# Optimization experiments

Hardware: AMD Instinct MI355X
Metric: run time of the kernel (lower is better)

## Reference

```python
import jax, jax.numpy as jnp
import numpy as np

L = 4            # n_layers
D_MODEL = 768
D_STATE = 16
D_CONV = 4
EXPAND = 2
D_INNER = EXPAND * D_MODEL      # 1536
DT_RANK = (D_MODEL + 15) // 16  # 48
B = 2
T = 2048
LN_EPS = 1e-5


def setup_inputs() -> dict:
    key = jax.random.key(0)
    ks = jax.random.split(key, 12)
    s = 0.02
    x = jax.random.normal(ks[0], (B, T, D_MODEL), dtype=jnp.float32)
    in_proj_w = jax.random.normal(ks[1], (L, 2 * D_INNER, D_MODEL), dtype=jnp.float32) * s
    conv_w = jax.random.normal(ks[2], (L, D_INNER, D_CONV), dtype=jnp.float32) * s
    conv_b = jnp.zeros((L, D_INNER), dtype=jnp.float32)
    x_proj_w = jax.random.normal(ks[3], (L, DT_RANK + 2 * D_STATE, D_INNER), dtype=jnp.float32) * s
    dt_proj_w = jax.random.normal(ks[4], (L, D_INNER, DT_RANK), dtype=jnp.float32) * s
    dt_proj_b = jax.random.normal(ks[5], (L, D_INNER), dtype=jnp.float32) * 0.1
    # Standard S4D-real init: A = -[1..d_state], stored as log
    A_log = jnp.log(jnp.broadcast_to(
        jnp.arange(1, D_STATE + 1, dtype=jnp.float32), (L, D_INNER, D_STATE)))
    D_param = jnp.ones((L, D_INNER), dtype=jnp.float32)
    out_proj_w = jax.random.normal(ks[6], (L, D_MODEL, D_INNER), dtype=jnp.float32) * s
    ln_g = jnp.ones((L, D_MODEL), dtype=jnp.float32)
    ln_b = jnp.zeros((L, D_MODEL), dtype=jnp.float32)
    return {"x": x, "in_proj_w": in_proj_w, "conv_w": conv_w, "conv_b": conv_b,
            "x_proj_w": x_proj_w, "dt_proj_w": dt_proj_w, "dt_proj_b": dt_proj_b,
            "A_log": A_log, "D_param": D_param, "out_proj_w": out_proj_w,
            "ln_g": ln_g, "ln_b": ln_b}


def _layernorm(x, g, b):
    mu = jnp.mean(x, axis=-1, keepdims=True)
    var = jnp.mean(jnp.square(x - mu), axis=-1, keepdims=True)
    return (x - mu) * jax.lax.rsqrt(var + LN_EPS) * g + b


def _mamba_layer(x, inw, convw, convb, xpw, dtw, dtb, A_log, Dp, outw):
    # x: [B,T,d_model]
    Tn = x.shape[1]
    xz = jnp.einsum('btd,ed->bte', x, inw)          # [B,T,2*d_inner]
    xin, z = jnp.split(xz, 2, axis=-1)              # each [B,T,d_inner]
    # causal depthwise conv1d over time (kernel d_conv)
    xp = jnp.pad(xin, ((0, 0), (D_CONV - 1, 0), (0, 0)))
    xc = convb
    for k in range(D_CONV):
        xc = xc + xp[:, k:k + Tn, :] * convw[:, k]
    xc = jax.nn.silu(xc)                            # [B,T,d_inner]
    dbl = jnp.einsum('bti,ei->bte', xc, xpw)        # [B,T,dt_rank+2*d_state]
    dt, Bs, Cs = jnp.split(dbl, [DT_RANK, DT_RANK + D_STATE], axis=-1)
    dt = jax.nn.softplus(jnp.einsum('btr,dr->btd', dt, dtw) + dtb)  # [B,T,d_inner]
    A = -jnp.exp(A_log)                             # [d_inner,d_state]
    dA = jnp.exp(jnp.einsum('btd,dn->btdn', dt, A))  # discretized A
    dBu = (dt * xc)[..., None] * Bs[:, :, None, :]   # [B,T,d_inner,d_state]

    def step(h, inp):
        dA_t, dBu_t, C_t = inp                      # [B,d,n],[B,d,n],[B,n]
        h = dA_t * h + dBu_t
        y = jnp.einsum('bdn,bn->bd', h, C_t)
        return h, y

    h0 = jnp.zeros((x.shape[0], D_INNER, D_STATE), x.dtype)
    _, ys = jax.lax.scan(step, h0,
                         (jnp.swapaxes(dA, 0, 1), jnp.swapaxes(dBu, 0, 1),
                          jnp.swapaxes(Cs, 0, 1)))
    y = jnp.swapaxes(ys, 0, 1) + xc * Dp            # skip connection D*u
    y = y * jax.nn.silu(z)                          # gate
    return jnp.einsum('bti,ei->bte', y, outw)       # [B,T,d_model]


def reference(x, in_proj_w, conv_w, conv_b, x_proj_w, dt_proj_w, dt_proj_b,
              A_log, D_param, out_proj_w, ln_g, ln_b):
    for l in range(L):
        residual = x
        h = _mamba_layer(x, in_proj_w[l], conv_w[l], conv_b[l], x_proj_w[l],
                         dt_proj_w[l], dt_proj_b[l], A_log[l], D_param[l],
                         out_proj_w[l])
        h = _layernorm(h, ln_g[l], ln_b[l])
        x = h + residual                            # dropout=0 -> identity
    return x
```

## Files before the change

### kernel.cpp

```cpp
#include <hip/hip_runtime.h>

#define T_LEN 2048
#define DM    768
#define DI    1536
#define DS    16
#define BB    2
#define NROWS (BB * T_LEN)
#define NCH   64
#define CLEN  32
#define NSEG  8
#define SEGC  8

#define OFF_DTB 0
#define OFF_A   6144
#define OFF_DP  104448
#define OFF_CW  110592
#define OFF_CB  135168
#define OFF_LG  141312
#define OFF_LB  144384
#define PRM_TOT 147456

typedef __attribute__((ext_vector_type(8))) short bh8;
typedef __attribute__((ext_vector_type(4))) float f32x4;

typedef const __attribute__((address_space(1))) void as1_void;
typedef __attribute__((address_space(3))) void as3_void;

__device__ __forceinline__ void glds16(const void* g, void* l) {
    __builtin_amdgcn_global_load_lds((as1_void*)g, (as3_void*)l, 16, 0, 0);
}

__device__ __forceinline__ float bf2f(unsigned short u) {
    return __uint_as_float(((unsigned)u) << 16);
}
__device__ __forceinline__ unsigned short f2bf(float f) {
    unsigned u = __float_as_uint(f);
    u += 0x7FFFu + ((u >> 16) & 1u);
    return (unsigned short)(u >> 16);
}

__device__ __forceinline__ void ld8(const void* p, long e0, int bf, float* v) {
    if (bf) {
        bh8 u = *(const bh8*)((const unsigned short*)p + e0);
#pragma unroll
        for (int j = 0; j < 8; ++j) v[j] = bf2f((unsigned short)u[j]);
    } else {
        const f32x4* q = (const f32x4*)((const float*)p + e0);
        f32x4 a = q[0], b = q[1];
#pragma unroll
        for (int j = 0; j < 4; ++j) { v[j] = a[j]; v[4 + j] = b[j]; }
    }
}

__device__ __forceinline__ void cp8(unsigned short* dst, long de0,
                                    const void* src, long se0, int bf) {
    if (bf) {
        *(bh8*)&dst[de0] = *(const bh8*)((const unsigned short*)src + se0);
    } else {
        const f32x4* q = (const f32x4*)((const float*)src + se0);
        f32x4 a = q[0], b = q[1];
        bh8 o;
#pragma unroll
        for (int j = 0; j < 4; ++j) { o[j] = (short)f2bf(a[j]); o[4 + j] = (short)f2bf(b[j]); }
        *(bh8*)&dst[de0] = o;
    }
}

__global__ void k_sniff(const unsigned short* __restrict__ x, int* __restrict__ flag) {
    __shared__ int cnt[4];
    int tid = threadIdx.x;
    int local = 0;
#pragma unroll
    for (int j = 0; j < 4; ++j) {
        unsigned short u = x[tid * 4 + j];
        int e = (u >> 7) & 0xFF;
        if (e >= 100 && e <= 140) local++;
    }
    for (int off = 32; off; off >>= 1) local += __shfl_down(local, off, 64);
    if ((tid & 63) == 0) cnt[tid >> 6] = local;
    __syncthreads();
    if (tid == 0) {
        int tot = cnt[0] + cnt[1] + cnt[2] + cnt[3];
        *flag = (tot >= 900) ? 1 : 0;
    }
}

__global__ void k_prep(const void* in_x, const void* in_inw, const void* in_ow,
                       const void* in_xpw, const void* in_dtw,
                       const void* dtb, const void* alog, const void* dpar,
                       const void* cw, const void* cb, const void* lg, const void* lb,
                       unsigned short* __restrict__ xbf, float* __restrict__ xf,
                       unsigned short* __restrict__ Win, unsigned short* __restrict__ Wout,
                       unsigned short* __restrict__ Wxp, unsigned short* __restrict__ Wdt,
                       float* __restrict__ prm, const int* __restrict__ flag) {
    const long G0 = 393216L;
    const long G1 = G0 + 1179648L;
    const long G2 = G1 + 589824L;
    const long G3 = G2 + 98304L;
    const long G4 = G3 + 49152L;
    const long G5 = G4 + 18432L;
    int bf = *flag;
    long g = (long)blockIdx.x * 256 + threadIdx.x;
    if (g >= G5) return;
    if (g < G0) {
        long e0 = g * 8;
        float v[8];
        ld8(in_x, e0, bf, v);
        bh8 o;
#pragma unroll
        for (int j = 0; j < 8; ++j) o[j] = (short)f2bf(v[j]);
        *(bh8*)&xbf[e0] = o;
        f32x4 a, b;
#pragma unroll
        for (int j = 0; j < 4; ++j) { a[j] = v[j]; b[j] = v[4 + j]; }
        ((f32x4*)&xf[e0])[0] = a;
        ((f32x4*)&xf[e0])[1] = b;
    } else if (g < G1) {
        long e0 = (g - G0) * 8;
        cp8(Win, e0, in_inw, e0, bf);
    } else if (g < G2) {
        long e0 = (g - G1) * 8;
        cp8(Wout, e0, in_ow, e0, bf);
    } else if (g < G3) {
        long e0 = (g - G2) * 8;
        int c = (int)(e0 % 1536);
        long rl = e0 / 1536;
        int r = (int)(rl % 128);
        int l = (int)(rl / 128);
        if (r < 80) cp8(Wxp, e0, in_xpw, ((long)l * 80 + r) * 1536 + c, bf);
        else        *(bh8*)&Wxp[e0] = (bh8)(short)0;
    } else if (g < G4) {
        long e0 = (g - G3) * 8;
        int c = (int)(e0 & 63);
        long rl = e0 >> 6;
        int d = (int)(rl % 1536);
        int l = (int)(rl / 1536);
        if (c < 48) cp8(Wdt, e0, in_dtw, ((long)l * 1536 + d) * 48 + c, bf);
        else        *(bh8*)&Wdt[e0] = (bh8)(short)0;
    } else {
        long e0 = (g - G4) * 8;
        float v[8];
        if (e0 < OFF_A)        ld8(dtb,  e0 - OFF_DTB, bf, v);
        else if (e0 < OFF_DP) {
            ld8(alog, e0 - OFF_A, bf, v);
#pragma unroll
            for (int j = 0; j < 8; ++j) v[j] = -__expf(v[j]);
        }
        else if (e0 < OFF_CW)  ld8(dpar, e0 - OFF_DP, bf, v);
        else if (e0 < OFF_CB)  ld8(cw,   e0 - OFF_CW, bf, v);
        else if (e0 < OFF_LG)  ld8(cb,   e0 - OFF_CB, bf, v);
        else if (e0 < OFF_LB)  ld8(lg,   e0 - OFF_LG, bf, v);
        else                   ld8(lb,   e0 - OFF_LB, bf, v);
        f32x4 a, b;
#pragma unroll
        for (int j = 0; j < 4; ++j) { a[j] = v[j]; b[j] = v[4 + j]; }
        ((f32x4*)&prm[e0])[0] = a;
        ((f32x4*)&prm[e0])[1] = b;
    }
}

template <int OUTF32>
__global__ __launch_bounds__(256) void k_gemm128(const unsigned short* __restrict__ A,
                                                 const unsigned short* __restrict__ B,
                                                 void* __restrict__ Cv,
                                                 int M, int N, int K) {
    __shared__ __align__(16) unsigned short As[128 * 32];
    __shared__ __align__(16) unsigned short Bs[128 * 32];
    const int tid = threadIdx.x;
    const int lane = tid & 63, wid = tid >> 6;
    const int wm = wid >> 1, wn = wid & 1;
    const long arow0 = (long)blockIdx.y * 128;
    const long bcol0 = (long)blockIdx.x * 128;
    const int r16 = lane >> 2;
    const int c8  = (lane & 3) * 8;
    f32x4 acc[4][4] = {};

    for (int k0 = 0; k0 < K; k0 += 32) {
#pragma unroll
        for (int j = 0; j < 2; ++j) {
            int chunk = wid + j * 4;
            int row = chunk * 16 + r16;
            glds16(&A[(arow0 + row) * K + k0 + c8], &As[chunk * 512]);
            glds16(&B[(bcol0 + row) * K + k0 + c8], &Bs[chunk * 512]);
        }
        __syncthreads();
        const int row = lane & 15, q8 = (lane >> 4) * 8;
        bh8 af[4], bfr[4];
#pragma unroll
        for (int i = 0; i < 4; ++i) af[i] = *(const bh8*)&As[(wm * 64 + i * 16 + row) * 32 + q8];
#pragma unroll
        for (int i = 0; i < 4; ++i) bfr[i] = *(const bh8*)&Bs[(wn * 64 + i * 16 + row) * 32 + q8];
#pragma unroll
        for (int i = 0; i < 4; ++i)
#pragma unroll
            for (int j = 0; j < 4; ++j)
                acc[i][j] = __builtin_amdgcn_mfma_f32_16x16x32_bf16(af[i], bfr[j], acc[i][j], 0, 0, 0);
        __syncthreads();
    }
    const int crow = (lane >> 4) * 4, ccol = lane & 15;
#pragma unroll
    for (int i = 0; i < 4; ++i)
#pragma unroll
        for (int j = 0; j < 4; ++j)
#pragma unroll
            for (int r = 0; r < 4; ++r) {
                long gr = arow0 + wm * 64 + i * 16 + crow + r;
                long gc = bcol0 + wn * 64 + j * 16 + ccol;
                if (OUTF32) ((float*)Cv)[gr * N + gc] = acc[i][j][r];
                else ((unsigned short*)Cv)[gr * N + gc] = f2bf(acc[i][j][r]);
            }
}

__global__ __launch_bounds__(256) void k_xproj(const unsigned short* __restrict__ A,
                                               const unsigned short* __restrict__ B,
                                               float* __restrict__ C) {
    __shared__ __align__(16) unsigned short As[32 * 32];
    __shared__ __align__(16) unsigned short Bs[64 * 32];
    const int tid = threadIdx.x;
    const int lane = tid & 63, w = tid >> 6;
    const int wm = w >> 1, wn = w & 1;
    const long arow0 = (long)blockIdx.y * 32;
    const long bcol0 = (long)blockIdx.x * 64;
    const int r4 = lane >> 2;
    const int c8 = (lane & 3) * 8;
    f32x4 acc[2] = {};

    for (int k0 = 0; k0 < DI; k0 += 32) {
        if (w < 2) {
            glds16(&A[(arow0 + w * 16 + r4) * DI + k0 + c8], &As[w * 512]);
            glds16(&B[(bcol0 + 32 + w * 16 + r4) * DI + k0 + c8], &Bs[1024 + w * 512]);
        } else {
            glds16(&B[(bcol0 + (w - 2) * 16 + r4) * DI + k0 + c8], &Bs[(w - 2) * 512]);
        }
        __syncthreads();
        const int row2 = lane & 15, q8 = (lane >> 4) * 8;
        bh8 af = *(const bh8*)&As[(wm * 16 + row2) * 32 + q8];
        bh8 b0 = *(const bh8*)&Bs[(wn * 32 + row2) * 32 + q8];
        bh8 b1 = *(const bh8*)&Bs[(wn * 32 + 16 + row2) * 32 + q8];
        acc[0] = __builtin_amdgcn_mfma_f32_16x16x32_bf16(af, b0, acc[0], 0, 0, 0);
        acc[1] = __builtin_amdgcn_mfma_f32_16x16x32_bf16(af, b1, acc[1], 0, 0, 0);
        __syncthreads();
    }
    const int crow = (lane >> 4) * 4, ccol = lane & 15;
#pragma unroll
    for (int j = 0; j < 2; ++j)
#pragma unroll
        for (int r = 0; r < 4; ++r) {
            long gr = arow0 + wm * 16 + crow + r;
            long gc = bcol0 + wn * 32 + j * 16 + ccol;
            C[gr * 128 + gc] = acc[j][r];
        }
}

__global__ __launch_bounds__(256) void k_dtproj(const float* __restrict__ Dbl,
                                                const unsigned short* __restrict__ Wdt,
                                                const float* __restrict__ bias,
                                                unsigned short* __restrict__ Dt) {
    __shared__ __align__(16) unsigned short As[2 * 64 * 32];
    __shared__ __align__(16) unsigned short Bs[2 * 64 * 32];
    const int tid = threadIdx.x;
    const int lane = tid & 63, wid = tid >> 6;
    const int wm = wid >> 1, wn = wid & 1;
    const long arow0 = (long)blockIdx.y * 64;
    const long bcol0 = (long)blockIdx.x * 64;

    {
        int r = tid >> 2;
        int cs = (tid & 3) * 16;
        unsigned short tmp[16];
#pragma unroll
        for (int q = 0; q < 4; ++q) {
            int col0 = cs + q * 4;
            if (col0 < 48) {
                f32x4 v = *(const f32x4*)&Dbl[(arow0 + r) * 128 + col0];
#pragma unroll
                for (int j = 0; j < 4; ++j) tmp[q * 4 + j] = f2bf(v[j]);
            } else {
#pragma unroll
                for (int j = 0; j < 4; ++j) tmp[q * 4 + j] = 0;
            }
        }
        int p = cs >> 5;
        int cp = cs & 31;
        *(bh8*)&As[p * 2048 + r * 32 + cp]     = *(bh8*)&tmp[0];
        *(bh8*)&As[p * 2048 + r * 32 + cp + 8] = *(bh8*)&tmp[8];
    }
#pragma unroll
    for (int j = 0; j < 2; ++j) {
        int chunk = tid + j * 256;
        int p = chunk >> 8;
        int rem = chunk & 255;
        int row = rem >> 2;
        int c4 = rem & 3;
        glds16(&Wdt[(bcol0 + row) * 64 + p * 32 + c4 * 8], &Bs[chunk * 8]);
    }
    __syncthreads();

    const int row2 = lane & 15, q8 = (lane >> 4) * 8;
    f32x4 acc[2][2] = {};
#pragma unroll
    for (int p = 0; p < 2; ++p) {
        bh8 af[2], bfr[2];
#pragma unroll
        for (int i = 0; i < 2; ++i) af[i] = *(const bh8*)&As[p * 2048 + (wm * 32 + i * 16 + row2) * 32 + q8];
#pragma unroll
        for (int i = 0; i < 2; ++i) bfr[i] = *(const bh8*)&Bs[p * 2048 + (wn * 32 + i * 16 + row2) * 32 + q8];
#pragma unroll
        for (int i = 0; i < 2; ++i)
#pragma unroll
            for (int j = 0; j < 2; ++j)
                acc[i][j] = __builtin_amdgcn_mfma_f32_16x16x32_bf16(af[i], bfr[j], acc[i][j], 0, 0, 0);
    }
    const int crow = (lane >> 4) * 4, ccol = lane & 15;
#pragma unroll
    for (int i = 0; i < 2; ++i)
#pragma unroll
        for (int j = 0; j < 2; ++j)
#pragma unroll
            for (int r = 0; r < 4; ++r) {
                long gr = arow0 + wm * 32 + i * 16 + crow + r;
                long gc = bcol0 + wn * 32 + j * 16 + ccol;
                float v = acc[i][j][r] + bias[gc];
                v = (v > 20.f) ? v : log1pf(__expf(v));
                Dt[gr * DI + gc] = f2bf(v);
            }
}

__global__ __launch_bounds__(256) void k_conv(const unsigned short* __restrict__ xz,
                                              const float* __restrict__ cw,
                                              const float* __restrict__ cb,
                                              unsigned short* __restrict__ xcbf) {
    __shared__ float tile[131 * 64];
    const int tid = threadIdx.x;
    const int d0 = blockIdx.x * 64;
    const long t0 = (long)blockIdx.y * 128;
    const bool seqstart = ((int)t0 & (T_LEN - 1)) == 0;
    for (int j = tid; j < 131 * 64; j += 256) {
        int row = j >> 6, col = j & 63;
        float v = 0.f;
        if (!(seqstart && row < 3)) v = bf2f(xz[(t0 - 3 + row) * (2 * DI) + d0 + col]);
        tile[j] = v;
    }
    __syncthreads();
    const int d = tid & 63, tl0 = tid >> 6;
    const int dg = d0 + d;
    const float w0 = cw[dg * 4 + 0], w1 = cw[dg * 4 + 1];
    const float w2 = cw[dg * 4 + 2], w3 = cw[dg * 4 + 3];
    const float bias = cb[dg];
    for (int tt = tl0; tt < 128; tt += 4) {
        float acc = bias + w0 * tile[tt * 64 + d] + w1 * tile[(tt + 1) * 64 + d]
                         + w2 * tile[(tt + 2) * 64 + d] + w3 * tile[(tt + 3) * 64 + d];
        float s = acc / (1.f + __expf(-acc));
        xcbf[(t0 + tt) * DI + dg] = f2bf(s);
    }
}

__global__ __launch_bounds__(256) void k_scan1(const unsigned short* __restrict__ dt,
                                               const unsigned short* __restrict__ xcbf,
                                               const float* __restrict__ dbl,
                                               const float* __restrict__ An,
                                               float* __restrict__ hch,
                                               float* __restrict__ sdtb) {
    const int tid = threadIdx.x;
    const int db = blockIdx.x % 6;
    const int c  = (blockIdx.x / 6) % NCH;
    const int b  = blockIdx.x / (6 * NCH);
    const int d  = db * 256 + tid;
    const int t0 = c * CLEN;
    float h[DS], An_r[DS];
    const f32x4* Ap = (const f32x4*)(An + (long)d * DS);
#pragma unroll
    for (int q = 0; q < 4; ++q) {
        f32x4 a4 = Ap[q];
#pragma unroll
        for (int j = 0; j < 4; ++j) { An_r[q * 4 + j] = a4[j]; h[q * 4 + j] = 0.f; }
    }
    float sdt = 0.f;
    const long rowb = (long)b * T_LEN + t0;
#pragma unroll 4
    for (int s = 0; s < CLEN; ++s) {
        long bt = rowb + s;
        float dtv = bf2f(dt[bt * DI + d]);
        float xcv = bf2f(xcbf[bt * DI + d]);
        int bi = __builtin_amdgcn_readfirstlane((int)(bt * 128 + 48));
        const f32x4* bp = (const f32x4*)(dbl + bi);
        float Bv[DS];
#pragma unroll
        for (int q = 0; q < 4; ++q) {
            f32x4 b4 = bp[q];
#pragma unroll
            for (int j = 0; j < 4; ++j) Bv[q * 4 + j] = b4[j];
        }
        float du = dtv * xcv;
        sdt += dtv;
#pragma unroll
        for (int n = 0; n < DS; ++n)
            h[n] = __expf(An_r[n] * dtv) * h[n] + du * Bv[n];
    }
    long o = (((long)b * NCH + c) * DI + d) * DS;
    f32x4* hp = (f32x4*)(hch + o);
#pragma unroll
    for (int q = 0; q < 4; ++q) {
        f32x4 h4;
#pragma unroll
        for (int j = 0; j < 4; ++j) h4[j] = h[q * 4 + j];
        hp[q] = h4;
    }
    sdtb[((long)b * NCH + c) * DI + d] = sdt;
}

__global__ __launch_bounds__(256) void k_scan2a(float* __restrict__ hbuf,
                                                const float* __restrict__ sdtb,
                                                const float* __restrict__ An,
                                                float* __restrict__ cum,
                                                float* __restrict__ Gseg,
                                                float* __restrict__ Sseg) {
    long gid = (long)blockIdx.x * 256 + threadIdx.x;
    int n = (int)(gid & 15);
    long t = gid >> 4;
    int d  = (int)(t % DI);
    int sg = (int)((t / DI) & (NSEG - 1));
    int b  = (int)(t / (DI * NSEG));
    float an = An[(long)d * DS + n];
    float h = 0.f, cs = 0.f;
    for (int i = 0; i < SEGC; ++i) {
        int c = sg * SEGC + i;
        long rowi = ((long)b * NCH + c) * DI + d;
        long idx = rowi * DS + n;
        float sdt = sdtb[rowi];
        float g = hbuf[idx];
        hbuf[idx] = h;
        if (n == 0) cum[rowi] = cs;
        h = __expf(an * sdt) * h + g;
        cs += sdt;
    }
    long gi = (((long)b * NSEG + sg) * DI + d) * DS + n;
    Gseg[gi] = h;
    if (n == 0) Sseg[((long)b * NSEG + sg) * DI + d] = cs;
}

__global__ __launch_bounds__(256) void k_scan2b(const float* __restrict__ Gseg,
                                                const float* __restrict__ Sseg,
                                                const float* __restrict__ An,
                                                float* __restrict__ Hseg) {
    long gid = (long)blockIdx.x * 256 + threadIdx.x;
    int n = (int)(gid & 15);
    long t = gid >> 4;
    int d = (int)(t % DI);
    int b = (int)(t / DI);
    float an = An[(long)d * DS + n];
    float H = 0.f;
    for (int sg = 0; sg < NSEG; ++sg) {
        long gi = (((long)b * NSEG + sg) * DI + d) * DS + n;
        float G = Gseg[gi];
        float S = Sseg[((long)b * NSEG + sg) * DI + d];
        Hseg[gi] = H;
        H = __expf(an * S) * H + G;
    }
}

__global__ __launch_bounds__(256) void k_scan3(const unsigned short* __restrict__ dt,
                                               const unsigned short* __restrict__ xcbf,
                                               const float* __restrict__ dbl,
                                               const float* __restrict__ An,
                                               const float* __restrict__ Dp,
                                               const float* __restrict__ hpref,
                                               const float* __restrict__ cum,
                                               const float* __restrict__ Hseg,
                                               const unsigned short* __restrict__ xz,
                                               unsigned short* __restrict__ ybf) {
    const int tid = threadIdx.x;
    const int db = blockIdx.x % 6;
    const int c  = (blockIdx.x / 6) % NCH;
    const int b  = blockIdx.x / (6 * NCH);
    const int d  = db * 256 + tid;
    const int t0 = c * CLEN;
    const int sg = c / SEGC;
    float h[DS], An_r[DS];
    long rowi = ((long)b * NCH + c) * DI + d;
    long o = rowi * DS;
    long gi = (((long)b * NSEG + sg) * DI + d) * DS;
    const float cs = cum[rowi];
    const f32x4* Ap = (const f32x4*)(An + (long)d * DS);
    const f32x4* Pp = (const f32x4*)(hpref + o);
    const f32x4* Hp = (const f32x4*)(Hseg + gi);
#pragma unroll
    for (int q = 0; q < 4; ++q) {
        f32x4 a4 = Ap[q], p4 = Pp[q], h4 = Hp[q];
#pragma unroll
        for (int j = 0; j < 4; ++j) {
            int n = q * 4 + j;
            An_r[n] = a4[j];
            h[n] = __expf(a4[j] * cs) * h4[j] + p4[j];
        }
    }
    const float dcoef = Dp[d];
    const long rowb = (long)b * T_LEN + t0;
#pragma unroll 4
    for (int s = 0; s < CLEN; ++s) {
        long bt = rowb + s;
        float dtv = bf2f(dt[bt * DI + d]);
        float xcv = bf2f(xcbf[bt * DI + d]);
        int bi = __builtin_amdgcn_readfirstlane((int)(bt * 128 + 48));
        const f32x4* bp = (const f32x4*)(dbl + bi);
        float Bv[DS], Cv[DS];
#pragma unroll
        for (int q = 0; q < 4; ++q) {
            f32x4 b4 = bp[q], c4 = bp[q + 4];
#pragma unroll
            for (int j = 0; j < 4; ++j) { Bv[q * 4 + j] = b4[j]; Cv[q * 4 + j] = c4[j]; }
        }
        float du = dtv * xcv;
        float yp[4] = {xcv * dcoef, 0.f, 0.f, 0.f};
#pragma unroll
        for (int n = 0; n < DS; ++n) {
            h[n] = __expf(An_r[n] * dtv) * h[n] + du * Bv[n];
            yp[n & 3] += h[n] * Cv[n];
        }
        float y = (yp[0] + yp[1]) + (yp[2] + yp[3]);
        float zv = bf2f(xz[bt * (2 * DI) + DI + d]);
        y *= zv / (1.f + __expf(-zv));
        ybf[bt * DI + d] = f2bf(y);
    }
}

__global__ __launch_bounds__(256) void k_ln(const float* __restrict__ prj,
                                            float* __restrict__ x,
                                            unsigned short* __restrict__ xbf,
                                            const float* __restrict__ lg,
                                            const float* __restrict__ lb,
                                            void* __restrict__ dout,
                                            int is_last, const int* __restrict__ flag) {
    __shared__ float red[8];
    const int row = blockIdx.x;
    const int tid = threadIdx.x;
    float v[3];
    float s = 0.f, s2 = 0.f;
#pragma unroll
    for (int j = 0; j < 3; ++j) {
        v[j] = prj[(long)row * DM + tid + j * 256];
        s += v[j];
        s2 += v[j] * v[j];
    }
    for (int off = 32; off; off >>= 1) {
        s  += __shfl_down(s, off, 64);
        s2 += __shfl_down(s2, off, 64);
    }
    if ((tid & 63) == 0) { red[tid >> 6] = s; red[4 + (tid >> 6)] = s2; }
    __syncthreads();
    float S  = red[0] + red[1] + red[2] + red[3];
    float S2 = red[4] + red[5] + red[6] + red[7];
    float mu = S * (1.f / DM);
    float var = S2 * (1.f / DM) - mu * mu;
    float rs = rsqrtf(var + 1e-5f);
    int bf = *flag;
#pragma unroll
    for (int j = 0; j < 3; ++j) {
        int e = tid + j * 256;
        long idx = (long)row * DM + e;
        float out = (v[j] - mu) * rs * lg[e] + lb[e] + x[idx];
        x[idx] = out;
        xbf[idx] = f2bf(out);
        if (is_last) {
            if (bf) ((unsigned short*)dout)[idx] = f2bf(out);
            else    ((float*)dout)[idx] = out;
        }
    }
}

extern "C" void kernel_launch(void* const* d_in, const int* in_sizes, int n_in,
                              void* d_out, int out_size, void* d_ws, size_t ws_size,
                              hipStream_t stream) {
    char* ws = (char*)d_ws;
    const size_t O_FLAG = 0;
    const size_t O_WIN  = 256;
    const size_t O_WXP  = O_WIN  + 18874368;
    const size_t O_WDT  = O_WXP  + 1572864;
    const size_t O_WOUT = O_WDT  + 786432;
    const size_t O_PRM  = O_WOUT + 9437184;
    const size_t O_XBF  = O_PRM  + 589824;
    const size_t O_XF   = O_XBF  + 6291456;
    const size_t O_XZ   = O_XF   + 12582912;
    const size_t O_XCBF = O_XZ   + 25165824;
    const size_t O_DBL  = O_XCBF + 12582912;
    const size_t O_DT   = O_DBL  + 2097152;
    const size_t O_HCH  = O_DT   + 12582912;
    const size_t O_SDT  = O_HCH  + 12582912;
    const size_t O_CUM  = O_SDT  + 786432;
    const size_t O_GSEG = O_CUM  + 786432;
    const size_t O_SSEG = O_GSEG + 1572864;
    const size_t O_HSEG = O_SSEG + 98304;
    const size_t O_YBF  = O_HSEG + 1572864;

    int* flag = (int*)(ws + O_FLAG);
    unsigned short* Win  = (unsigned short*)(ws + O_WIN);
    unsigned short* Wxp  = (unsigned short*)(ws + O_WXP);
    unsigned short* Wdt  = (unsigned short*)(ws + O_WDT);
    unsigned short* Wout = (unsigned short*)(ws + O_WOUT);
    float* prm = (float*)(ws + O_PRM);
    unsigned short* Xbf = (unsigned short*)(ws + O_XBF);
    float* Xf  = (float*)(ws + O_XF);
    unsigned short* Xz = (unsigned short*)(ws + O_XZ);
    unsigned short* Xcbf = (unsigned short*)(ws + O_XCBF);
    float* Dbl = (float*)(ws + O_DBL);
    unsigned short* Dt = (unsigned short*)(ws + O_DT);
    float* Hch = (float*)(ws + O_HCH);
    float* Sdt = (float*)(ws + O_SDT);
    float* Cum = (float*)(ws + O_CUM);
    float* Gsg = (float*)(ws + O_GSEG);
    float* Ssg = (float*)(ws + O_SSEG);
    float* Hsg = (float*)(ws + O_HSEG);
    unsigned short* Ybf = (unsigned short*)(ws + O_YBF);
    float* Prj = (float*)(ws + O_XZ);

    k_sniff<<<1, 256, 0, stream>>>((const unsigned short*)d_in[0], flag);
    k_prep<<<9096, 256, 0, stream>>>(d_in[0], d_in[1], d_in[9], d_in[4], d_in[5],
                                     d_in[6], d_in[7], d_in[8], d_in[2], d_in[3],
                                     d_in[10], d_in[11],
                                     Xbf, Xf, Win, Wout, Wxp, Wdt, prm, flag);

    for (int l = 0; l < 4; ++l) {
        const unsigned short* winL  = Win  + (size_t)l * 3072 * 768;
        const unsigned short* wxpL  = Wxp  + (size_t)l * 128 * 1536;
        const unsigned short* wdtL  = Wdt  + (size_t)l * 1536 * 64;
        const unsigned short* woutL = Wout + (size_t)l * 768 * 1536;
        const float* cwL  = prm + OFF_CW  + (size_t)l * DI * 4;
        const float* cbL  = prm + OFF_CB  + (size_t)l * DI;
        const float* dtbL = prm + OFF_DTB + (size_t)l * DI;
        const float* anL  = prm + OFF_A   + (size_t)l * DI * DS;
        const float* dpL  = prm + OFF_DP  + (size_t)l * DI;
        const float* lgL  = prm + OFF_LG  + (size_t)l * DM;
        const float* lbL  = prm + OFF_LB  + (size_t)l * DM;

        k_gemm128<0><<<dim3(24, 32), 256, 0, stream>>>(Xbf, winL, Xz, NROWS, 2 * DI, DM);
        k_conv<<<dim3(24, 32), 256, 0, stream>>>(Xz, cwL, cbL, Xcbf);
        k_xproj<<<dim3(2, 128), 256, 0, stream>>>(Xcbf, wxpL, Dbl);
        k_dtproj<<<dim3(24, 64), 256, 0, stream>>>(Dbl, wdtL, dtbL, Dt);
        k_scan1<<<BB * NCH * 6, 256, 0, stream>>>(Dt, Xcbf, Dbl, anL, Hch, Sdt);
        k_scan2a<<<1536, 256, 0, stream>>>(Hch, Sdt, anL, Cum, Gsg, Ssg);
        k_scan2b<<<192, 256, 0, stream>>>(Gsg, Ssg, anL, Hsg);
        k_scan3<<<BB * NCH * 6, 256, 0, stream>>>(Dt, Xcbf, Dbl, anL, dpL, Hch, Cum, Hsg, Xz, Ybf);
        k_gemm128<1><<<dim3(6, 32), 256, 0, stream>>>(Ybf, woutL, Prj, NROWS, DM, DI);
        k_ln<<<4096, 256, 0, stream>>>(Prj, Xf, Xbf, lgL, lbL, d_out, (l == 3) ? 1 : 0, flag);
    }
}
```

Before: 948.9 us.

## Fuse causal conv into x_proj and scans, drop scan2b, split-K x_proj

Removes the standalone conv kernel and its intermediate buffer. The causal depthwise conv plus SiLU is now recomputed inside x_proj, which also gains a split-K over 4 z-slices accumulated with atomics, and inside both scan kernels from the raw xz buffer. scan2b is eliminated: scan3 recombines the per-segment carries itself in a short serial loop. Scan chunks are halved and their count doubled for more parallelism, and out_proj gets a dedicated 64x64-tile GEMM for more blocks. The cost is redundant conv math, atomic float adds with nondeterministic summation order, and a memset per layer.

Result: slower. 969.1 us (+2.1%).

```diff
diff --git a/kernel.cpp b/kernel.cpp
--- a/kernel.cpp
+++ b/kernel.cpp
@@ -6,10 +6,10 @@
 #define DS    16
 #define BB    2
 #define NROWS (BB * T_LEN)
-#define NCH   64
-#define CLEN  32
+#define NCH   128
+#define CLEN  16
 #define NSEG  8
-#define SEGC  8
+#define SEGC  16
 
 #define OFF_DTB 0
 #define OFF_A   6144
@@ -159,10 +159,9 @@
     }
 }
 
-template <int OUTF32>
 __global__ __launch_bounds__(256) void k_gemm128(const unsigned short* __restrict__ A,
                                                  const unsigned short* __restrict__ B,
-                                                 void* __restrict__ Cv,
+                                                 unsigned short* __restrict__ C,
                                                  int M, int N, int K) {
     __shared__ __align__(16) unsigned short As[128 * 32];
     __shared__ __align__(16) unsigned short Bs[128 * 32];
@@ -206,50 +205,81 @@
             for (int r = 0; r < 4; ++r) {
                 long gr = arow0 + wm * 64 + i * 16 + crow + r;
                 long gc = bcol0 + wn * 64 + j * 16 + ccol;
-                if (OUTF32) ((float*)Cv)[gr * N + gc] = acc[i][j][r];
-                else ((unsigned short*)Cv)[gr * N + gc] = f2bf(acc[i][j][r]);
+                C[gr * N + gc] = f2bf(acc[i][j][r]);
             }
 }
 
-__global__ __launch_bounds__(256) void k_xproj(const unsigned short* __restrict__ A,
+__global__ __launch_bounds__(256) void k_xproj(const unsigned short* __restrict__ xz,
                                                const unsigned short* __restrict__ B,
+                                               const float* __restrict__ cw,
+                                               const float* __restrict__ cb,
                                                float* __restrict__ C) {
-    __shared__ __align__(16) unsigned short As[32 * 32];
+    __shared__ __align__(16) unsigned short As[64 * 32];
     __shared__ __align__(16) unsigned short Bs[64 * 32];
     const int tid = threadIdx.x;
     const int lane = tid & 63, w = tid >> 6;
     const int wm = w >> 1, wn = w & 1;
-    const long arow0 = (long)blockIdx.y * 32;
+    const long arow0 = (long)blockIdx.y * 64;
     const long bcol0 = (long)blockIdx.x * 64;
+    const int kbase = blockIdx.z * 384;
     const int r4 = lane >> 2;
     const int c8 = (lane & 3) * 8;
-    f32x4 acc[2] = {};
-
-    for (int k0 = 0; k0 < DI; k0 += 32) {
-        if (w < 2) {
-            glds16(&A[(arow0 + w * 16 + r4) * DI + k0 + c8], &As[w * 512]);
-            glds16(&B[(bcol0 + 32 + w * 16 + r4) * DI + k0 + c8], &Bs[1024 + w * 512]);
-        } else {
-            glds16(&B[(bcol0 + (w - 2) * 16 + r4) * DI + k0 + c8], &Bs[(w - 2) * 512]);
-        }
+    const int t_o = tid >> 2;
+    const int dl  = (tid & 3) * 8;
+    const int sp  = (int)((arow0 + t_o) & (T_LEN - 1));
+    f32x4 acc[2][2] = {};
+
+    for (int kk = 0; kk < 384; kk += 32) {
+        const int k0 = kbase + kk;
+        glds16(&B[(bcol0 + w * 16 + r4) * DI + k0 + c8], &Bs[w * 512]);
+        const int dg = k0 + dl;
+        float xv[4][8];
+#pragma unroll
+        for (int rr = 0; rr < 4; ++rr) {
+            if (sp - 3 + rr >= 0) {
+                bh8 u = *(const bh8*)&xz[(arow0 + t_o - 3 + rr) * 3072 + dg];
+#pragma unroll
+                for (int q = 0; q < 8; ++q) xv[rr][q] = bf2f((unsigned short)u[q]);
+            } else {
+#pragma unroll
+                for (int q = 0; q < 8; ++q) xv[rr][q] = 0.f;
+            }
+        }
+        bh8 o;
+#pragma unroll
+        for (int q = 0; q < 8; ++q) {
+            const f32x4 w4 = *(const f32x4*)&cw[(dg + q) * 4];
+            float a = cb[dg + q] + w4[0] * xv[0][q] + w4[1] * xv[1][q]
+                                 + w4[2] * xv[2][q] + w4[3] * xv[3][q];
+            a = a / (1.f + __expf(-a));
+            o[q] = (short)f2bf(a);
+        }
+        *(bh8*)&As[t_o * 32 + dl] = o;
         __syncthreads();
         const int row2 = lane & 15, q8 = (lane >> 4) * 8;
-        bh8 af = *(const bh8*)&As[(wm * 16 + row2) * 32 + q8];
-        bh8 b0 = *(const bh8*)&Bs[(wn * 32 + row2) * 32 + q8];
-        bh8 b1 = *(const bh8*)&Bs[(wn * 32 + 16 + row2) * 32 + q8];
-        acc[0] = __builtin_amdgcn_mfma_f32_16x16x32_bf16(af, b0, acc[0], 0, 0, 0);
-        acc[1] = __builtin_amdgcn_mfma_f32_16x16x32_bf16(af, b1, acc[1], 0, 0, 0);
+        bh8 af[2], bfr[2];
+#pragma unroll
+        for (int i = 0; i < 2; ++i) af[i] = *(const bh8*)&As[(wm * 32 + i * 16 + row2) * 32 + q8];
+#pragma unroll
+        for (int i = 0; i < 2; ++i) bfr[i] = *(const bh8*)&Bs[(wn * 32 + i * 16 + row2) * 32 + q8];
+#pragma unroll
+        for (int i = 0; i < 2; ++i)
+#pragma unroll
+            for (int j = 0; j < 2; ++j)
+                acc[i][j] = __builtin_amdgcn_mfma_f32_16x16x32_bf16(af[i], bfr[j], acc[i][j], 0, 0, 0);
         __syncthreads();
     }
     const int crow = (lane >> 4) * 4, ccol = lane & 15;
 #pragma unroll
-    for (int j = 0; j < 2; ++j)
-#pragma unroll
-        for (int r = 0; r < 4; ++r) {
-            long gr = arow0 + wm * 16 + crow + r;
-            long gc = bcol0 + wn * 32 + j * 16 + ccol;
-            C[gr * 128 + gc] = acc[j][r];
-        }
+    for (int i = 0; i < 2; ++i)
+#pragma unroll
+        for (int j = 0; j < 2; ++j)
+#pragma unroll
+            for (int r = 0; r < 4; ++r) {
+                long gr = arow0 + wm * 32 + i * 16 + crow + r;
+                long gc = bcol0 + wn * 32 + j * 16 + ccol;
+                atomicAdd(&C[gr * 128 + gc], acc[i][j][r]);
+            }
 }
 
 __global__ __launch_bounds__(256) void k_dtproj(const float* __restrict__ Dbl,
@@ -326,39 +356,57 @@
             }
 }
 
-__global__ __launch_bounds__(256) void k_conv(const unsigned short* __restrict__ xz,
-                                              const float* __restrict__ cw,
-                                              const float* __restrict__ cb,
-                                              unsigned short* __restrict__ xcbf) {
-    __shared__ float tile[131 * 64];
+__global__ __launch_bounds__(256) void k_outproj(const unsigned short* __restrict__ A,
+                                                 const unsigned short* __restrict__ B,
+                                                 float* __restrict__ C) {
+    __shared__ __align__(16) unsigned short As[64 * 32];
+    __shared__ __align__(16) unsigned short Bs[64 * 32];
     const int tid = threadIdx.x;
-    const int d0 = blockIdx.x * 64;
-    const long t0 = (long)blockIdx.y * 128;
-    const bool seqstart = ((int)t0 & (T_LEN - 1)) == 0;
-    for (int j = tid; j < 131 * 64; j += 256) {
-        int row = j >> 6, col = j & 63;
-        float v = 0.f;
-        if (!(seqstart && row < 3)) v = bf2f(xz[(t0 - 3 + row) * (2 * DI) + d0 + col]);
-        tile[j] = v;
-    }
-    __syncthreads();
-    const int d = tid & 63, tl0 = tid >> 6;
-    const int dg = d0 + d;
-    const float w0 = cw[dg * 4 + 0], w1 = cw[dg * 4 + 1];
-    const float w2 = cw[dg * 4 + 2], w3 = cw[dg * 4 + 3];
-    const float bias = cb[dg];
-    for (int tt = tl0; tt < 128; tt += 4) {
-        float acc = bias + w0 * tile[tt * 64 + d] + w1 * tile[(tt + 1) * 64 + d]
-                         + w2 * tile[(tt + 2) * 64 + d] + w3 * tile[(tt + 3) * 64 + d];
-        float s = acc / (1.f + __expf(-acc));
-        xcbf[(t0 + tt) * DI + dg] = f2bf(s);
-    }
+    const int lane = tid & 63, wid = tid >> 6;
+    const int wm = wid >> 1, wn = wid & 1;
+    const long arow0 = (long)blockIdx.y * 64;
+    const long bcol0 = (long)blockIdx.x * 64;
+    const int r16 = lane >> 2;
+    const int c8  = (lane & 3) * 8;
+    f32x4 acc[2][2] = {};
+
+    for (int k0 = 0; k0 < DI; k0 += 32) {
+        int row = wid * 16 + r16;
+        glds16(&A[(arow0 + row) * DI + k0 + c8], &As[wid * 512]);
+        glds16(&B[(bcol0 + row) * DI + k0 + c8], &Bs[wid * 512]);
+        __syncthreads();
+        const int row2 = lane & 15, q8 = (lane >> 4) * 8;
+        bh8 af[2], bfr[2];
+#pragma unroll
+        for (int i = 0; i < 2; ++i) af[i] = *(const bh8*)&As[(wm * 32 + i * 16 + row2) * 32 + q8];
+#pragma unroll
+        for (int i = 0; i < 2; ++i) bfr[i] = *(const bh8*)&Bs[(wn * 32 + i * 16 + row2) * 32 + q8];
+#pragma unroll
+        for (int i = 0; i < 2; ++i)
+#pragma unroll
+            for (int j = 0; j < 2; ++j)
+                acc[i][j] = __builtin_amdgcn_mfma_f32_16x16x32_bf16(af[i], bfr[j], acc[i][j], 0, 0, 0);
+        __syncthreads();
+    }
+    const int crow = (lane >> 4) * 4, ccol = lane & 15;
+#pragma unroll
+    for (int i = 0; i < 2; ++i)
+#pragma unroll
+        for (int j = 0; j < 2; ++j)
+#pragma unroll
+            for (int r = 0; r < 4; ++r) {
+                long gr = arow0 + wm * 32 + i * 16 + crow + r;
+                long gc = bcol0 + wn * 32 + j * 16 + ccol;
+                C[gr * DM + gc] = acc[i][j][r];
+            }
 }
 
 __global__ __launch_bounds__(256) void k_scan1(const unsigned short* __restrict__ dt,
-                                               const unsigned short* __restrict__ xcbf,
+                                               const unsigned short* __restrict__ xz,
                                                const float* __restrict__ dbl,
                                                const float* __restrict__ An,
+                                               const float* __restrict__ cw,
+                                               const float* __restrict__ cb,
                                                float* __restrict__ hch,
                                                float* __restrict__ sdtb) {
     const int tid = threadIdx.x;
@@ -375,13 +423,25 @@
 #pragma unroll
         for (int j = 0; j < 4; ++j) { An_r[q * 4 + j] = a4[j]; h[q * 4 + j] = 0.f; }
     }
+    const f32x4 w4 = *(const f32x4*)&cw[d * 4];
+    const float cbv = cb[d];
+    const long rowb = (long)b * T_LEN + t0;
+    float x1, x2, x3;
+    if (c == 0) { x1 = x2 = x3 = 0.f; }
+    else {
+        x1 = bf2f(xz[(rowb - 1) * 3072 + d]);
+        x2 = bf2f(xz[(rowb - 2) * 3072 + d]);
+        x3 = bf2f(xz[(rowb - 3) * 3072 + d]);
+    }
     float sdt = 0.f;
-    const long rowb = (long)b * T_LEN + t0;
 #pragma unroll 4
     for (int s = 0; s < CLEN; ++s) {
         long bt = rowb + s;
+        float xt = bf2f(xz[bt * 3072 + d]);
+        float a = cbv + w4[0] * x3 + w4[1] * x2 + w4[2] * x1 + w4[3] * xt;
+        float xcv = a / (1.f + __expf(-a));
+        x3 = x2; x2 = x1; x1 = xt;
         float dtv = bf2f(dt[bt * DI + d]);
-        float xcv = bf2f(xcbf[bt * DI + d]);
         int bi = __builtin_amdgcn_readfirstlane((int)(bt * 128 + 48));
         const f32x4* bp = (const f32x4*)(dbl + bi);
         float Bv[DS];
@@ -439,35 +499,17 @@
     if (n == 0) Sseg[((long)b * NSEG + sg) * DI + d] = cs;
 }
 
-__global__ __launch_bounds__(256) void k_scan2b(const float* __restrict__ Gseg,
-                                                const float* __restrict__ Sseg,
-                                                const float* __restrict__ An,
-                                                float* __restrict__ Hseg) {
-    long gid = (long)blockIdx.x * 256 + threadIdx.x;
-    int n = (int)(gid & 15);
-    long t = gid >> 4;
-    int d = (int)(t % DI);
-    int b = (int)(t / DI);
-    float an = An[(long)d * DS + n];
-    float H = 0.f;
-    for (int sg = 0; sg < NSEG; ++sg) {
-        long gi = (((long)b * NSEG + sg) * DI + d) * DS + n;
-        float G = Gseg[gi];
-        float S = Sseg[((long)b * NSEG + sg) * DI + d];
-        Hseg[gi] = H;
-        H = __expf(an * S) * H + G;
-    }
-}
-
 __global__ __launch_bounds__(256) void k_scan3(const unsigned short* __restrict__ dt,
-                                               const unsigned short* __restrict__ xcbf,
+                                               const unsigned short* __restrict__ xz,
                                                const float* __restrict__ dbl,
                                                const float* __restrict__ An,
+                                               const float* __restrict__ cw,
+                                               const float* __restrict__ cb,
                                                const float* __restrict__ Dp,
                                                const float* __restrict__ hpref,
                                                const float* __restrict__ cum,
-                                               const float* __restrict__ Hseg,
-                                               const unsigned short* __restrict__ xz,
+                                               const float* __restrict__ Gseg,
+                                               const float* __restrict__ Sseg,
                                                unsigned short* __restrict__ ybf) {
     const int tid = threadIdx.x;
     const int db = blockIdx.x % 6;
@@ -479,28 +521,60 @@
     float h[DS], An_r[DS];
     long rowi = ((long)b * NCH + c) * DI + d;
     long o = rowi * DS;
-    long gi = (((long)b * NSEG + sg) * DI + d) * DS;
     const float cs = cum[rowi];
     const f32x4* Ap = (const f32x4*)(An + (long)d * DS);
+#pragma unroll
+    for (int q = 0; q < 4; ++q) {
+        f32x4 a4 = Ap[q];
+#pragma unroll
+        for (int j = 0; j < 4; ++j) An_r[q * 4 + j] = a4[j];
+    }
+    float Hn[DS];
+#pragma unroll
+    for (int n = 0; n < DS; ++n) Hn[n] = 0.f;
+    for (int s2 = 0; s2 < sg; ++s2) {
+        long gi = (((long)b * NSEG + s2) * DI + d) * DS;
+        float S = Sseg[((long)b * NSEG + s2) * DI + d];
+        const f32x4* Gp = (const f32x4*)(Gseg + gi);
+#pragma unroll
+        for (int q = 0; q < 4; ++q) {
+            f32x4 g4 = Gp[q];
+#pragma unroll
+            for (int j = 0; j < 4; ++j) {
+                int n = q * 4 + j;
+                Hn[n] = __expf(An_r[n] * S) * Hn[n] + g4[j];
+            }
+        }
+    }
     const f32x4* Pp = (const f32x4*)(hpref + o);
-    const f32x4* Hp = (const f32x4*)(Hseg + gi);
 #pragma unroll
     for (int q = 0; q < 4; ++q) {
-        f32x4 a4 = Ap[q], p4 = Pp[q], h4 = Hp[q];
+        f32x4 p4 = Pp[q];
 #pragma unroll
         for (int j = 0; j < 4; ++j) {
             int n = q * 4 + j;
-            An_r[n] = a4[j];
-            h[n] = __expf(a4[j] * cs) * h4[j] + p4[j];
+            h[n] = __expf(An_r[n] * cs) * Hn[n] + p4[j];
         }
     }
     const float dcoef = Dp[d];
+    const f32x4 w4 = *(const f32x4*)&cw[d * 4];
+    const float cbv = cb[d];
     const long rowb = (long)b * T_LEN + t0;
+    float x1, x2, x3;
+    if (c == 0) { x1 = x2 = x3 = 0.f; }
+    else {
+        x1 = bf2f(xz[(rowb - 1) * 3072 + d]);
+        x2 = bf2f(xz[(rowb - 2) * 3072 + d]);
+        x3 = bf2f(xz[(rowb - 3) * 3072 + d]);
+    }
 #pragma unroll 4
     for (int s = 0; s < CLEN; ++s) {
         long bt = rowb + s;
+        float xt = bf2f(xz[bt * 3072 + d]);
+        float a = cbv + w4[0] * x3 + w4[1] * x2 + w4[2] * x1 + w4[3] * xt;
+        float xcv = a / (1.f + __expf(-a));
+        x3 = x2; x2 = x1; x1 = xt;
         float dtv = bf2f(dt[bt * DI + d]);
-        float xcv = bf2f(xcbf[bt * DI + d]);
         int bi = __builtin_amdgcn_readfirstlane((int)(bt * 128 + 48));
         const f32x4* bp = (const f32x4*)(dbl + bi);
         float Bv[DS], Cv[DS];
@@ -518,7 +592,7 @@
             yp[n & 3] += h[n] * Cv[n];
         }
         float y = (yp[0] + yp[1]) + (yp[2] + yp[3]);
-        float zv = bf2f(xz[bt * (2 * DI) + DI + d]);
+        float zv = bf2f(xz[bt * 3072 + DI + d]);
         y *= zv / (1.f + __expf(-zv));
         ybf[bt * DI + d] = f2bf(y);
     }
@@ -581,16 +655,14 @@
     const size_t O_XBF  = O_PRM  + 589824;
     const size_t O_XF   = O_XBF  + 6291456;
     const size_t O_XZ   = O_XF   + 12582912;
-    const size_t O_XCBF = O_XZ   + 25165824;
-    const size_t O_DBL  = O_XCBF + 12582912;
+    const size_t O_DBL  = O_XZ   + 25165824;
     const size_t O_DT   = O_DBL  + 2097152;
     const size_t O_HCH  = O_DT   + 12582912;
-    const size_t O_SDT  = O_HCH  + 12582912;
-    const size_t O_CUM  = O_SDT  + 786432;
-    const size_t O_GSEG = O_CUM  + 786432;
+    const size_t O_SDT  = O_HCH  + 25165824;
+    const size_t O_CUM  = O_SDT  + 1572864;
+    const size_t O_GSEG = O_CUM  + 1572864;
     const size_t O_SSEG = O_GSEG + 1572864;
-    const size_t O_HSEG = O_SSEG + 98304;
-    const size_t O_YBF  = O_HSEG + 1572864;
+    const size_t O_YBF  = O_SSEG + 98304;
 
     int* flag = (int*)(ws + O_FLAG);
     unsigned short* Win  = (unsigned short*)(ws + O_WIN);
@@ -601,7 +673,6 @@
     unsigned short* Xbf = (unsigned short*)(ws + O_XBF);
     float* Xf  = (float*)(ws + O_XF);
     unsigned short* Xz = (unsigned short*)(ws + O_XZ);
-    unsigned short* Xcbf = (unsigned short*)(ws + O_XCBF);
     float* Dbl = (float*)(ws + O_DBL);
     unsigned short* Dt = (unsigned short*)(ws + O_DT);
     float* Hch = (float*)(ws + O_HCH);
@@ -609,7 +680,6 @@
     float* Cum = (float*)(ws + O_CUM);
     float* Gsg = (float*)(ws + O_GSEG);
     float* Ssg = (float*)(ws + O_SSEG);
-    float* Hsg = (float*)(ws + O_HSEG);
     unsigned short* Ybf = (unsigned short*)(ws + O_YBF);
     float* Prj = (float*)(ws + O_XZ);
 
@@ -632,15 +702,15 @@
         const float* lgL  = prm + OFF_LG  + (size_t)l * DM;
         const float* lbL  = prm + OFF_LB  + (size_t)l * DM;
 
-        k_gemm128<0><<<dim3(24, 32), 256, 0, stream>>>(Xbf, winL, Xz, NROWS, 2 * DI, DM);
-        k_conv<<<dim3(24, 32), 256, 0, stream>>>(Xz, cwL, cbL, Xcbf);
-        k_xproj<<<dim3(2, 128), 256, 0, stream>>>(Xcbf, wxpL, Dbl);
+        k_gemm128<<<dim3(24, 32), 256, 0, stream>>>(Xbf, winL, Xz, NROWS, 2 * DI, DM);
+        hipMemsetAsync(Dbl, 0, 2097152, stream);
+        k_xproj<<<dim3(2, 64, 4), 256, 0, stream>>>(Xz, wxpL, cwL, cbL, Dbl);
         k_dtproj<<<dim3(24, 64), 256, 0, stream>>>(Dbl, wdtL, dtbL, Dt);
-        k_scan1<<<BB * NCH * 6, 256, 0, stream>>>(Dt, Xcbf, Dbl, anL, Hch, Sdt);
+        k_scan1<<<BB * NCH * 6, 256, 0, stream>>>(Dt, Xz, Dbl, anL, cwL, cbL, Hch, Sdt);
         k_scan2a<<<1536, 256, 0, stream>>>(Hch, Sdt, anL, Cum, Gsg, Ssg);
-        k_scan2b<<<192, 256, 0, stream>>>(Gsg, Ssg, anL, Hsg);
-        k_scan3<<<BB * NCH * 6, 256, 0, stream>>>(Dt, Xcbf, Dbl, anL, dpL, Hch, Cum, Hsg, Xz, Ybf);
-        k_gemm128<1><<<dim3(6, 32), 256, 0, stream>>>(Ybf, woutL, Prj, NROWS, DM, DI);
+        k_scan3<<<BB * NCH * 6, 256, 0, stream>>>(Dt, Xz, Dbl, anL, cwL, cbL, dpL,
+                                                  Hch, Cum, Gsg, Ssg, Ybf);
+        k_outproj<<<dim3(12, 64), 256, 0, stream>>>(Ybf, woutL, Prj);
         k_ln<<<4096, 256, 0, stream>>>(Prj, Xf, Xbf, lgL, lbL, d_out, (l == 3) ? 1 : 0, flag);
     }
 }
```
